# Optimization experiments

Measured on AMD Instinct MI355X. Metric: run time of the kernel, lower is better.

Reference implementation:

```python
import jax, jax.numpy as jnp
import numpy as np

M = 1024  # input_size
D = 1024  # output_size
Q_SCALE = 0.06  # hardcoded scale in original module (not 1/sqrt(d))


def setup_inputs() -> dict:
    key = jax.random.key(0)
    kx, kk, kq, kv, ko = jax.random.split(key, 5)
    n = 4096
    s = 1.0 / np.sqrt(M)
    x = jax.random.normal(kx, (n, M), dtype=jnp.float32)
    # nn.Linear(bias=False): y = x @ W.T with W [out,in]; store as [in,out]
    Wk = jax.random.uniform(kk, (M, D), jnp.float32, -s, s)
    Wq = jax.random.uniform(kq, (M, D), jnp.float32, -s, s)
    Wv = jax.random.uniform(kv, (M, D), jnp.float32, -s, s)
    Wo = jax.random.uniform(ko, (D, M), jnp.float32, -1.0 / np.sqrt(D), 1.0 / np.sqrt(D))
    return {"x": x, "Wk": Wk, "Wq": Wq, "Wv": Wv, "Wo": Wo}


def reference(x, Wk, Wq, Wv, Wo):
    K = x @ Wk                      # [n, D]
    Q = (x @ Wq) * Q_SCALE          # [n, D]
    V = x @ Wv                      # [n, D]
    logits = Q @ K.T                # [n, n]
    att = jax.nn.softmax(logits, axis=-1)
    # dropout in eval mode = identity
    y = att @ V                     # [n, D]
    return y @ Wo                   # [n, M]
```

## Files before the change

### kernel.cpp

```cpp
#include <hip/hip_runtime.h>
#include <hip/hip_bf16.h>
#include <stdint.h>

using bf16 = __hip_bfloat16;
typedef __attribute__((ext_vector_type(8))) short short8;
typedef __attribute__((ext_vector_type(4))) float f32x4;
typedef __attribute__((ext_vector_type(4))) unsigned short u16x4;

__device__ __forceinline__ float bf2f(short u) {
  unsigned int b = ((unsigned int)(unsigned short)u) << 16;
  return __builtin_bit_cast(float, b);
}
__device__ __forceinline__ unsigned short f2bf(float f) {
  unsigned int u = __builtin_bit_cast(unsigned int, f);
  u += 0x7fffu + ((u >> 16) & 1u);
  return (unsigned short)(u >> 16);
}

__device__ __forceinline__ void gload_lds16(const bf16* g, bf16* l) {
  __builtin_amdgcn_global_load_lds(
      (const __attribute__((address_space(1))) void*)g,
      (__attribute__((address_space(3))) void*)l, 16, 0, 0);
}

#define SCHED0 __builtin_amdgcn_sched_barrier(0)
#define BAR do { SCHED0; __builtin_amdgcn_s_barrier(); SCHED0; } while (0)
#define LGKM0 do { asm volatile("s_waitcnt lgkmcnt(0)" ::: "memory"); SCHED0; } while (0)
#define VMCNT6 asm volatile("s_waitcnt vmcnt(6)" ::: "memory")


template <int BUF, int Q>
__device__ __forceinline__ void lds_A(const char* sm, int rbA, int sl0, int sl1,
                                      short8 (&aF)[4][2]) {
#pragma unroll
  for (int mi = 0; mi < 4; ++mi) {
    const char* p = sm + BUF * 65536 + rbA + (Q * 64 + mi * 16) * 128;
    aF[mi][0] = *(const short8*)(p + sl0);
    aF[mi][1] = *(const short8*)(p + sl1);
  }
}
template <int BUF, int H>
__device__ __forceinline__ void lds_B(const char* sm, int rbB, int sl0, int sl1,
                                      short8 (&bF)[2][2]) {
#pragma unroll
  for (int ni = 0; ni < 2; ++ni) {
    const char* p = sm + BUF * 65536 + rbB + (H * 32 + ni * 16) * 128;
    bF[ni][0] = *(const short8*)(p + sl0);
    bF[ni][1] = *(const short8*)(p + sl1);
  }
}
template <int Q, int H>
__device__ __forceinline__ void mfma_q(short8 (&aF)[4][2], short8 (&bF)[2][2],
                                       f32x4 (&acc)[8][4]) {
  __builtin_amdgcn_s_setprio(1);
#pragma unroll
  for (int mi = 0; mi < 4; ++mi)
#pragma unroll
    for (int ni = 0; ni < 2; ++ni)
#pragma unroll
      for (int kk = 0; kk < 2; ++kk)
        acc[Q * 4 + mi][H * 2 + ni] = __builtin_amdgcn_mfma_f32_16x16x32_bf16(
            aF[mi][kk], bF[ni][kk], acc[Q * 4 + mi][H * 2 + ni], 0, 0, 0);
  __builtin_amdgcn_s_setprio(0);
}

template <typename OutT, int TAG>
__global__ __launch_bounds__(512, 2)
void gemm256(const bf16* __restrict__ A, int lda,
             const bf16* __restrict__ Bt, int ldb,
             OutT* __restrict__ C, int ldc, int K, size_t splitStride) {
  __shared__ __align__(16) char sm[131072];
  const int kz = blockIdx.z * K;
  A += kz;
  Bt += kz;
  C += (size_t)blockIdx.z * splitStride;

  const int tid = threadIdx.x;
  const int wid = tid >> 6;
  const int lane = tid & 63;
  const int m0 = blockIdx.y * 256;
  const int n0 = blockIdx.x * 256;
  const int NT = K >> 6;
  const int NI = NT >> 1;

  const int sr = tid >> 3;
  const int scs = ((tid & 7) ^ (sr & 7)) << 3;
  const bf16* Ag = A + (size_t)(m0 + sr) * lda + scs;
  const bf16* Bg = Bt + (size_t)(n0 + sr) * ldb + scs;
  const int stW = wid * 8 * 128;

  const int lr = lane & 15;
  const int rbA = ((wid >> 2) * 128 + lr) * 128;
  const int rbB = 32768 + ((wid & 3) * 64 + lr) * 128;
  const int sl0 = (((lane >> 4) ^ (lane & 7)) << 4);
  const int sl1 = ((((lane >> 4) + 4) ^ (lane & 7)) << 4);

  f32x4 acc[8][4] = {};
  short8 aF[4][2], b0F[2][2], b1F[2][2];

  auto stageA = [&](int buf, int tile, int half) {
    const bf16* s = Ag + (size_t)(half * 128) * lda + tile * 64;
    char* d = sm + buf * 65536 + (half * 128) * 128 + stW;
    gload_lds16(s, (bf16*)d);
    gload_lds16(s + (size_t)64 * lda, (bf16*)(d + 64 * 128));
  };
  auto stageB = [&](int buf, int tile, int half) {
    const bf16* s = Bg + (size_t)(half * 128) * ldb + tile * 64;
    char* d = sm + buf * 65536 + 32768 + (half * 128) * 128 + stW;
    gload_lds16(s, (bf16*)d);
    gload_lds16(s + (size_t)64 * ldb, (bf16*)(d + 64 * 128));
  };

  stageA(0, 0, 0); stageA(0, 0, 1); stageB(0, 0, 0); stageB(0, 0, 1);
  stageB(1, 1, 0); stageB(1, 1, 1); stageA(1, 1, 0);
  VMCNT6;
  BAR;

  for (int i = 0; i < NI; ++i) {
    const int t1 = 2 * i + 1;
    const int t2 = (2 * i + 2 < NT) ? 2 * i + 2 : NT - 1;
    const int t3 = (2 * i + 3 < NT) ? 2 * i + 3 : NT - 1;
    lds_A<0, 0>(sm, rbA, sl0, sl1, aF);
    lds_B<0, 0>(sm, rbB, sl0, sl1, b0F);
    stageA(1, t1, 1);
    BAR; LGKM0; mfma_q<0, 0>(aF, b0F, acc); BAR;
    lds_B<0, 1>(sm, rbB, sl0, sl1, b1F);
    BAR; LGKM0; mfma_q<0, 1>(aF, b1F, acc); BAR;
    lds_A<0, 1>(sm, rbA, sl0, sl1, aF);
    stageB(0, t2, 0);
    BAR; LGKM0; mfma_q<1, 1>(aF, b1F, acc); BAR;
    stageB(0, t2, 1); stageA(0, t2, 0);
    VMCNT6;
    BAR; mfma_q<1, 0>(aF, b0F, acc); BAR;
    lds_A<1, 0>(sm, rbA, sl0, sl1, aF);
    lds_B<1, 0>(sm, rbB, sl0, sl1, b0F);
    stageA(0, t2, 1);
    BAR; LGKM0; mfma_q<0, 0>(aF, b0F, acc); BAR;
    lds_B<1, 1>(sm, rbB, sl0, sl1, b1F);
    BAR; LGKM0; mfma_q<0, 1>(aF, b1F, acc); BAR;
    lds_A<1, 1>(sm, rbA, sl0, sl1, aF);
    stageB(1, t3, 0);
    BAR; LGKM0; mfma_q<1, 1>(aF, b1F, acc); BAR;
    stageB(1, t3, 1); stageA(1, t3, 0);
    VMCNT6;
    BAR; mfma_q<1, 0>(aF, b0F, acc); BAR;
  }

  const int cr = (lane >> 4) * 4;
  const int cc = lane & 15;
  const int wm = (wid >> 2) * 128;
  const int wn = (wid & 3) * 64;
#pragma unroll
  for (int mi = 0; mi < 8; ++mi)
#pragma unroll
    for (int ni = 0; ni < 4; ++ni) {
      const int row = m0 + wm + mi * 16 + cr;
      const int col = n0 + wn + ni * 16 + cc;
#pragma unroll
      for (int j = 0; j < 4; ++j) {
        float v = acc[mi][ni][j];
        if constexpr (sizeof(OutT) == 2)
          ((unsigned short*)C)[(size_t)(row + j) * ldc + col] = f2bf(v);
        else
          C[(size_t)(row + j) * ldc + col] = v;
      }
    }
}

template <typename OutT, int TAG>
__global__ __launch_bounds__(256)
void gemm_bt(const bf16* __restrict__ A, int lda,
             const bf16* __restrict__ Bt, int ldb,
             OutT* __restrict__ C, int ldc, int K, size_t splitStride) {
  constexpr int BK = 64;
  __shared__ __align__(16) bf16 As[128 * BK];
  __shared__ __align__(16) bf16 Bs[128 * BK];

  const int kz = blockIdx.z * K;
  A += kz;
  Bt += kz;
  C += (size_t)blockIdx.z * splitStride;

  const int tid = threadIdx.x;
  const int wid = tid >> 6;
  const int lane = tid & 63;
  const int m0 = blockIdx.y * 128;
  const int n0 = blockIdx.x * 128;

  const int arow = tid >> 3;
  const int acol = (tid & 7) * 8;
  const int lr = lane & 15;
  const int lk = (lane >> 4) * 8;
  const int wm = (wid >> 1) * 64;
  const int wn = (wid & 1) * 64;

  const bf16* Ag = A + (size_t)(m0 + arow) * lda + acol;
  const bf16* Bg = Bt + (size_t)(n0 + arow) * ldb + acol;
  bf16* Asw = As + wid * 512;
  bf16* Bsw = Bs + wid * 512;

  f32x4 acc[4][4] = {};

  for (int kt = 0; kt < K; kt += BK) {
    __syncthreads();
#pragma unroll
    for (int r = 0; r < 4; ++r) {
      gload_lds16(Ag + (size_t)(r * 32) * lda + kt, Asw + r * 2048);
      gload_lds16(Bg + (size_t)(r * 32) * ldb + kt, Bsw + r * 2048);
    }
    __syncthreads();
#pragma unroll
    for (int kk = 0; kk < BK; kk += 32) {
      short8 a[4], b[4];
#pragma unroll
      for (int i = 0; i < 4; ++i)
        a[i] = *(const short8*)&As[(wm + i * 16 + lr) * BK + kk + lk];
#pragma unroll
      for (int i = 0; i < 4; ++i)
        b[i] = *(const short8*)&Bs[(wn + i * 16 + lr) * BK + kk + lk];
#pragma unroll
      for (int mi = 0; mi < 4; ++mi)
#pragma unroll
        for (int ni = 0; ni < 4; ++ni)
          acc[mi][ni] = __builtin_amdgcn_mfma_f32_16x16x32_bf16(
              a[mi], b[ni], acc[mi][ni], 0, 0, 0);
    }
  }

  const int cr = (lane >> 4) * 4;
  const int cc = lane & 15;
#pragma unroll
  for (int mi = 0; mi < 4; ++mi)
#pragma unroll
    for (int ni = 0; ni < 4; ++ni) {
      const int row = m0 + wm + mi * 16 + cr;
      const int col = n0 + wn + ni * 16 + cc;
#pragma unroll
      for (int j = 0; j < 4; ++j) {
        float v = acc[mi][ni][j];
        if constexpr (sizeof(OutT) == 2)
          ((unsigned short*)C)[(size_t)(row + j) * ldc + col] = f2bf(v);
        else
          C[(size_t)(row + j) * ldc + col] = v;
      }
    }
}

__global__ __launch_bounds__(256)
void reduce4_bf16(const unsigned short* __restrict__ p,
                  unsigned short* __restrict__ yb, int n) {
  const int i = (blockIdx.x * 256 + threadIdx.x) * 8;
  if (i >= n) return;
  const size_t st = (size_t)n;
  short8 a = *(const short8*)&p[i];
  short8 b = *(const short8*)&p[i + st];
  short8 c = *(const short8*)&p[i + 2 * st];
  short8 d = *(const short8*)&p[i + 3 * st];
  short8 o;
#pragma unroll
  for (int j = 0; j < 8; ++j)
    o[j] = (short)f2bf(bf2f(a[j]) + bf2f(b[j]) + bf2f(c[j]) + bf2f(d[j]));
  *(short8*)&yb[i] = o;
}

__global__ __launch_bounds__(256)
void softmax_rows(bf16* __restrict__ S) {
  unsigned short* p = (unsigned short*)(S + (size_t)blockIdx.x * 4096);
  const int tid = threadIdx.x;
  const int lane = tid & 63;
  const int wid = tid >> 6;

  short8 s0 = *(const short8*)&p[tid * 16];
  short8 s1 = *(const short8*)&p[tid * 16 + 8];
  float v[16];
#pragma unroll
  for (int i = 0; i < 8; ++i) v[i] = bf2f(s0[i]);
#pragma unroll
  for (int i = 0; i < 8; ++i) v[8 + i] = bf2f(s1[i]);

  float mx = v[0];
#pragma unroll
  for (int i = 1; i < 16; ++i) mx = fmaxf(mx, v[i]);
  for (int off = 32; off > 0; off >>= 1) mx = fmaxf(mx, __shfl_xor(mx, off));
  __shared__ float redm[4], reds[4];
  if (lane == 0) redm[wid] = mx;
  __syncthreads();
  mx = fmaxf(fmaxf(redm[0], redm[1]), fmaxf(redm[2], redm[3]));

  float sum = 0.f;
#pragma unroll
  for (int i = 0; i < 16; ++i) { v[i] = __expf(v[i] - mx); sum += v[i]; }
  for (int off = 32; off > 0; off >>= 1) sum += __shfl_xor(sum, off);
  if (lane == 0) reds[wid] = sum;
  __syncthreads();
  sum = reds[0] + reds[1] + reds[2] + reds[3];
  const float inv = 1.f / sum;

  short8 o0, o1;
#pragma unroll
  for (int i = 0; i < 8; ++i) o0[i] = (short)f2bf(v[i] * inv);
#pragma unroll
  for (int i = 0; i < 8; ++i) o1[i] = (short)f2bf(v[8 + i] * inv);
  *(short8*)&p[tid * 16] = o0;
  *(short8*)&p[tid * 16 + 8] = o1;
}

__global__ __launch_bounds__(256)
void tr_f32_bf16(const float* __restrict__ src, int ld,
                 unsigned short* __restrict__ dst, int dld, float scale) {
  __shared__ float t[32][33];
  const int bx = blockIdx.x * 32;
  const int by = blockIdx.y * 32;
  const int tx = threadIdx.x, ty = threadIdx.y;
#pragma unroll
  for (int j = 0; j < 4; ++j)
    t[ty + j * 8][tx] = src[(size_t)(by + ty + j * 8) * ld + bx + tx];
  __syncthreads();
#pragma unroll
  for (int j = 0; j < 4; ++j)
    dst[(size_t)(bx + ty + j * 8) * dld + by + tx] = f2bf(t[tx][ty + j * 8] * scale);
}

__global__ __launch_bounds__(256)
void tr_bf16(const unsigned short* __restrict__ src, int ld,
             unsigned short* __restrict__ dst, int dld) {
  __shared__ unsigned short t[32][33];
  const int bx = blockIdx.x * 32;
  const int by = blockIdx.y * 32;
  const int tx = threadIdx.x, ty = threadIdx.y;
#pragma unroll
  for (int j = 0; j < 4; ++j)
    t[ty + j * 8][tx] = src[(size_t)(by + ty + j * 8) * ld + bx + tx];
  __syncthreads();
#pragma unroll
  for (int j = 0; j < 4; ++j)
    dst[(size_t)(bx + ty + j * 8) * dld + by + tx] = t[tx][ty + j * 8];
}

__global__ __launch_bounds__(256)
void cvt_f32_bf16(const float* __restrict__ src, unsigned short* __restrict__ dst, int n) {
  const int i = (blockIdx.x * 256 + threadIdx.x) * 4;
  if (i >= n) return;
  f32x4 v = *(const f32x4*)&src[i];
  u16x4 o;
#pragma unroll
  for (int j = 0; j < 4; ++j) o[j] = f2bf(v[j]);
  *(u16x4*)&dst[i] = o;
}

extern "C" void kernel_launch(void* const* d_in, const int* in_sizes, int n_in,
                              void* d_out, int out_size, void* d_ws, size_t ws_size,
                              hipStream_t stream) {
  const float* x = (const float*)d_in[0];
  const float* Wk = (const float*)d_in[1];
  const float* Wq = (const float*)d_in[2];
  const float* Wv = (const float*)d_in[3];
  const float* Wo = (const float*)d_in[4];
  float* out = (float*)d_out;

  bf16* xb  = (bf16*)d_ws;
  bf16* Wt  = xb + (size_t)4096 * 1024;
  bf16* KQV = Wt + (size_t)3072 * 1024;
  bf16* Wot = KQV + (size_t)4096 * 3072;
  bf16* Vt  = Wot + (size_t)1024 * 1024;
  bf16* S   = Vt + (size_t)1024 * 4096;
  bf16* p4  = xb;
  bf16* yb  = S;

  const dim3 tb(32, 8);

  cvt_f32_bf16<<<dim3(4096), dim3(256), 0, stream>>>(x, (unsigned short*)xb, 4096 * 1024);
  tr_f32_bf16<<<dim3(32, 32), tb, 0, stream>>>(Wk, 1024, (unsigned short*)Wt, 1024, 1.0f);
  tr_f32_bf16<<<dim3(32, 32), tb, 0, stream>>>(Wq, 1024, (unsigned short*)(Wt + (size_t)1024 * 1024), 1024, 0.06f);
  tr_f32_bf16<<<dim3(32, 32), tb, 0, stream>>>(Wv, 1024, (unsigned short*)(Wt + (size_t)2048 * 1024), 1024, 1.0f);
  tr_f32_bf16<<<dim3(32, 32), tb, 0, stream>>>(Wo, 1024, (unsigned short*)Wot, 1024, 1.0f);

  gemm256<bf16, 0><<<dim3(12, 16, 1), dim3(512), 0, stream>>>(
      xb, 1024, Wt, 1024, KQV, 3072, 1024, 0);

  tr_bf16<<<dim3(32, 128), tb, 0, stream>>>((const unsigned short*)(KQV + 2048), 3072,
                                            (unsigned short*)Vt, 4096);

  gemm256<bf16, 1><<<dim3(16, 16, 1), dim3(512), 0, stream>>>(
      KQV + 1024, 3072, KQV, 3072, S, 4096, 1024, 0);

  softmax_rows<<<dim3(4096), dim3(256), 0, stream>>>(S);

  gemm256<bf16, 2><<<dim3(4, 16, 4), dim3(512), 0, stream>>>(
      S, 4096, Vt, 4096, p4, 1024, 1024, (size_t)4096 * 1024);

  reduce4_bf16<<<dim3(2048), dim3(256), 0, stream>>>(
      (const unsigned short*)p4, (unsigned short*)yb, 4096 * 1024);

  gemm_bt<float, 3><<<dim3(8, 32, 1), dim3(256), 0, stream>>>(
      yb, 1024, Wot, 1024, out, 1024, 1024, 0);
}
```

Baseline: 170.1 us.

## Switch 256x256 GEMM to 32x32x16 MFMA tiles and relax scheduling barriers

Replaces the 16x16x32 bf16 MFMA micro-tiles in the 256x256 GEMM with 32x32x16 MFMAs. The LDS fragment loads, accumulator layout (f32x16) and epilogue index mapping are reworked to match, and the K sub-steps are split differently between the four phases. The larger MFMA shape is meant to cut the number of MFMA issues and LDS fragment reads per tile. The sched_barrier fences around s_barrier are also removed, which gives the compiler more freedom to reorder code but risks moving loads across the phase boundaries.

```diff
diff --git a/kernel.cpp b/kernel.cpp
--- a/kernel.cpp
+++ b/kernel.cpp
@@ -5,6 +5,7 @@
 using bf16 = __hip_bfloat16;
 typedef __attribute__((ext_vector_type(8))) short short8;
 typedef __attribute__((ext_vector_type(4))) float f32x4;
+typedef __attribute__((ext_vector_type(16))) float f32x16;
 typedef __attribute__((ext_vector_type(4))) unsigned short u16x4;
 
 __device__ __forceinline__ float bf2f(short u) {
@@ -23,44 +24,46 @@
       (__attribute__((address_space(3))) void*)l, 16, 0, 0);
 }
 
-#define SCHED0 __builtin_amdgcn_sched_barrier(0)
-#define BAR do { SCHED0; __builtin_amdgcn_s_barrier(); SCHED0; } while (0)
-#define LGKM0 do { asm volatile("s_waitcnt lgkmcnt(0)" ::: "memory"); SCHED0; } while (0)
+#define BAR __builtin_amdgcn_s_barrier()
+#define LGKM0 do { asm volatile("s_waitcnt lgkmcnt(0)" ::: "memory"); \
+                   __builtin_amdgcn_sched_barrier(0); } while (0)
 #define VMCNT6 asm volatile("s_waitcnt vmcnt(6)" ::: "memory")
 
 
 template <int BUF, int Q>
-__device__ __forceinline__ void lds_A(const char* sm, int rbA, int sl0, int sl1,
-                                      short8 (&aF)[4][2]) {
-#pragma unroll
-  for (int mi = 0; mi < 4; ++mi) {
-    const char* p = sm + BUF * 65536 + rbA + (Q * 64 + mi * 16) * 128;
-    aF[mi][0] = *(const short8*)(p + sl0);
-    aF[mi][1] = *(const short8*)(p + sl1);
+__device__ __forceinline__ void lds_A32(const char* sm, int rbA, const int (&sl)[4],
+                                        short8 (&aF)[2][4]) {
+#pragma unroll
+  for (int mi = 0; mi < 2; ++mi) {
+    const char* p = sm + BUF * 65536 + rbA + (Q * 64 + mi * 32) * 128;
+#pragma unroll
+    for (int ks = 0; ks < 4; ++ks)
+      aF[mi][ks] = *(const short8*)(p + sl[ks]);
   }
 }
-template <int BUF, int H>
-__device__ __forceinline__ void lds_B(const char* sm, int rbB, int sl0, int sl1,
-                                      short8 (&bF)[2][2]) {
+template <int BUF, int KS>
+__device__ __forceinline__ void lds_B32(const char* sm, int rbB, const int (&sl)[4],
+                                        short8 (&bF)[2][2]) {
 #pragma unroll
   for (int ni = 0; ni < 2; ++ni) {
-    const char* p = sm + BUF * 65536 + rbB + (H * 32 + ni * 16) * 128;
-    bF[ni][0] = *(const short8*)(p + sl0);
-    bF[ni][1] = *(const short8*)(p + sl1);
+    const char* p = sm + BUF * 65536 + rbB + (ni * 32) * 128;
+#pragma unroll
+    for (int k2 = 0; k2 < 2; ++k2)
+      bF[ni][k2] = *(const short8*)(p + sl[KS * 2 + k2]);
   }
 }
-template <int Q, int H>
-__device__ __forceinline__ void mfma_q(short8 (&aF)[4][2], short8 (&bF)[2][2],
-                                       f32x4 (&acc)[8][4]) {
+template <int Q, int KS>
+__device__ __forceinline__ void mfma32(short8 (&aF)[2][4], short8 (&bF)[2][2],
+                                       f32x16 (&acc)[4][2]) {
   __builtin_amdgcn_s_setprio(1);
 #pragma unroll
-  for (int mi = 0; mi < 4; ++mi)
-#pragma unroll
-    for (int ni = 0; ni < 2; ++ni)
-#pragma unroll
-      for (int kk = 0; kk < 2; ++kk)
-        acc[Q * 4 + mi][H * 2 + ni] = __builtin_amdgcn_mfma_f32_16x16x32_bf16(
-            aF[mi][kk], bF[ni][kk], acc[Q * 4 + mi][H * 2 + ni], 0, 0, 0);
+  for (int k2 = 0; k2 < 2; ++k2)
+#pragma unroll
+    for (int mi = 0; mi < 2; ++mi)
+#pragma unroll
+      for (int ni = 0; ni < 2; ++ni)
+        acc[Q * 2 + mi][ni] = __builtin_amdgcn_mfma_f32_32x32x16_bf16(
+            aF[mi][KS * 2 + k2], bF[ni][k2], acc[Q * 2 + mi][ni], 0, 0, 0);
   __builtin_amdgcn_s_setprio(0);
 }
 
@@ -89,14 +92,17 @@
   const bf16* Bg = Bt + (size_t)(n0 + sr) * ldb + scs;
   const int stW = wid * 8 * 128;
 
-  const int lr = lane & 15;
-  const int rbA = ((wid >> 2) * 128 + lr) * 128;
-  const int rbB = 32768 + ((wid & 3) * 64 + lr) * 128;
-  const int sl0 = (((lane >> 4) ^ (lane & 7)) << 4);
-  const int sl1 = ((((lane >> 4) + 4) ^ (lane & 7)) << 4);
-
-  f32x4 acc[8][4] = {};
-  short8 aF[4][2], b0F[2][2], b1F[2][2];
+  const int lr32 = lane & 31;
+  const int hi = lane >> 5;
+  const int rbA = ((wid >> 2) * 128 + lr32) * 128;
+  const int rbB = 32768 + ((wid & 3) * 64 + lr32) * 128;
+  int sl[4];
+#pragma unroll
+  for (int ks = 0; ks < 4; ++ks)
+    sl[ks] = ((ks * 2 + hi) ^ (lane & 7)) << 4;
+
+  f32x16 acc[4][2] = {};
+  short8 aF[2][4], b0F[2][2], b1F[2][2];
 
   auto stageA = [&](int buf, int tile, int half) {
     const bf16* s = Ag + (size_t)(half * 128) * lda + tile * 64;
@@ -120,49 +126,50 @@
     const int t1 = 2 * i + 1;
     const int t2 = (2 * i + 2 < NT) ? 2 * i + 2 : NT - 1;
     const int t3 = (2 * i + 3 < NT) ? 2 * i + 3 : NT - 1;
-    lds_A<0, 0>(sm, rbA, sl0, sl1, aF);
-    lds_B<0, 0>(sm, rbB, sl0, sl1, b0F);
+    lds_A32<0, 0>(sm, rbA, sl, aF);
+    lds_B32<0, 0>(sm, rbB, sl, b0F);
     stageA(1, t1, 1);
-    BAR; LGKM0; mfma_q<0, 0>(aF, b0F, acc); BAR;
-    lds_B<0, 1>(sm, rbB, sl0, sl1, b1F);
-    BAR; LGKM0; mfma_q<0, 1>(aF, b1F, acc); BAR;
-    lds_A<0, 1>(sm, rbA, sl0, sl1, aF);
+    BAR; LGKM0; mfma32<0, 0>(aF, b0F, acc); BAR;
+    lds_B32<0, 1>(sm, rbB, sl, b1F);
+    BAR; LGKM0; mfma32<0, 1>(aF, b1F, acc); BAR;
+    lds_A32<0, 1>(sm, rbA, sl, aF);
     stageB(0, t2, 0);
-    BAR; LGKM0; mfma_q<1, 1>(aF, b1F, acc); BAR;
+    BAR; LGKM0; mfma32<1, 1>(aF, b1F, acc); BAR;
     stageB(0, t2, 1); stageA(0, t2, 0);
     VMCNT6;
-    BAR; mfma_q<1, 0>(aF, b0F, acc); BAR;
-    lds_A<1, 0>(sm, rbA, sl0, sl1, aF);
-    lds_B<1, 0>(sm, rbB, sl0, sl1, b0F);
+    BAR; mfma32<1, 0>(aF, b0F, acc); BAR;
+    lds_A32<1, 0>(sm, rbA, sl, aF);
+    lds_B32<1, 0>(sm, rbB, sl, b0F);
     stageA(0, t2, 1);
-    BAR; LGKM0; mfma_q<0, 0>(aF, b0F, acc); BAR;
-    lds_B<1, 1>(sm, rbB, sl0, sl1, b1F);
-    BAR; LGKM0; mfma_q<0, 1>(aF, b1F, acc); BAR;
-    lds_A<1, 1>(sm, rbA, sl0, sl1, aF);
+    BAR; LGKM0; mfma32<0, 0>(aF, b0F, acc); BAR;
+    lds_B32<1, 1>(sm, rbB, sl, b1F);
+    BAR; LGKM0; mfma32<0, 1>(aF, b1F, acc); BAR;
+    lds_A32<1, 1>(sm, rbA, sl, aF);
     stageB(1, t3, 0);
-    BAR; LGKM0; mfma_q<1, 1>(aF, b1F, acc); BAR;
+    BAR; LGKM0; mfma32<1, 1>(aF, b1F, acc); BAR;
     stageB(1, t3, 1); stageA(1, t3, 0);
     VMCNT6;
-    BAR; mfma_q<1, 0>(aF, b0F, acc); BAR;
+    BAR; mfma32<1, 0>(aF, b0F, acc); BAR;
   }
 
-  const int cr = (lane >> 4) * 4;
-  const int cc = lane & 15;
+  const int er = hi * 4;
+  const int ec = lr32;
   const int wm = (wid >> 2) * 128;
   const int wn = (wid & 3) * 64;
 #pragma unroll
-  for (int mi = 0; mi < 8; ++mi)
-#pragma unroll
-    for (int ni = 0; ni < 4; ++ni) {
-      const int row = m0 + wm + mi * 16 + cr;
-      const int col = n0 + wn + ni * 16 + cc;
-#pragma unroll
-      for (int j = 0; j < 4; ++j) {
-        float v = acc[mi][ni][j];
+  for (int qmi = 0; qmi < 4; ++qmi)
+#pragma unroll
+    for (int ni = 0; ni < 2; ++ni) {
+      const int row0 = m0 + wm + qmi * 32 + er;
+      const int col = n0 + wn + ni * 32 + ec;
+#pragma unroll
+      for (int reg = 0; reg < 16; ++reg) {
+        const int row = row0 + (reg & 3) + 8 * (reg >> 2);
+        float v = acc[qmi][ni][reg];
         if constexpr (sizeof(OutT) == 2)
-          ((unsigned short*)C)[(size_t)(row + j) * ldc + col] = f2bf(v);
+          ((unsigned short*)C)[(size_t)row * ldc + col] = f2bf(v);
         else
-          C[(size_t)(row + j) * ldc + col] = v;
+          C[(size_t)row * ldc + col] = v;
       }
     }
 }
```

Result: slower. 177.2 us (+4.2%).
